# Performance work log

Measured on AMD Instinct MI355X. Metric: run time of the kernel, lower is better.

Reference implementation:

```python
import jax, jax.numpy as jnp
import numpy as np
from jax import lax

B, IMG, ED, NC = 32, 224, 256, 10
DI, DS, DC, DR = 512, 64, 4, 16   # d_inner, d_state, d_conv, dt_rank
NB, L = 6, (IMG // 16) ** 2       # 6 mamba blocks, seq len 196
EPS = 1e-5


def setup_inputs():
    key = jax.random.key(0)
    ks = iter(jax.random.split(key, 48))
    def rn(shape, s=0.02):
        return jax.random.normal(next(ks), shape, jnp.float32) * s
    def ru(shape):
        return jax.random.uniform(next(ks), shape, jnp.float32, 0.5, 1.5)
    inp = {"x": jax.random.normal(next(ks), (B, 3, IMG, IMG), jnp.float32)}
    c = [ED // 4, ED // 2, ED]
    for i, (ci, co) in enumerate([(3, c[0]), (c[0], c[1]), (c[1], c[2])], 1):
        inp[f"c{i}w"] = rn((co, ci, 3, 3), 0.05)
        inp[f"c{i}b"] = rn((co,))
        inp[f"b{i}g"] = jnp.ones((co,), jnp.float32)
        inp[f"b{i}b"] = jnp.zeros((co,), jnp.float32)
        inp[f"b{i}m"] = rn((co,))
        inp[f"b{i}v"] = ru((co,))
    inp["ln_g"] = jnp.ones((NB, ED), jnp.float32)
    inp["ln_b"] = jnp.zeros((NB, ED), jnp.float32)
    inp["w_in"] = rn((NB, 2 * DI, ED))
    inp["cw"] = rn((NB, DI, DC), 0.1)
    inp["cb"] = rn((NB, DI))
    inp["w_x"] = rn((NB, DR + 2 * DS, DI))
    inp["w_dt"] = rn((NB, DI, DR), 0.1)
    inp["b_dt"] = rn((NB, DI), 0.5)
    inp["a_log"] = jnp.tile(jnp.log(jnp.arange(1, DS + 1, dtype=jnp.float32)), (NB, DI, 1))
    inp["d_skip"] = jnp.ones((NB, DI), jnp.float32)
    inp["w_out"] = rn((NB, ED, DI))
    inp["fc_w"] = rn((NC, ED))
    inp["fc_b"] = jnp.zeros((NC,), jnp.float32)
    return inp


def _conv2d(x, w, s, p):
    return lax.conv_general_dilated(x, w, (s, s), [(p, p), (p, p)],
                                    dimension_numbers=("NCHW", "OIHW", "NCHW"))


def _bn(x, g, b, m, v):
    sh = (1, -1, 1, 1)
    return (x - m.reshape(sh)) * (g.reshape(sh) / jnp.sqrt(v.reshape(sh) + EPS)) + b.reshape(sh)


def _maxpool(x, k, s, p):
    return lax.reduce_window(x, -jnp.inf, lax.max, (1, 1, k, k), (1, 1, s, s),
                             [(0, 0), (0, 0), (p, p), (p, p)])


def _mamba_block(x, ln_g, ln_b, w_in, cw, cb, w_x, w_dt, b_dt, a_log, d_skip, w_out):
    res = x
    mu = x.mean(-1, keepdims=True)
    var = ((x - mu) ** 2).mean(-1, keepdims=True)
    h = (x - mu) / jnp.sqrt(var + EPS) * ln_g + ln_b
    xz = jnp.einsum("bld,ed->ble", h, w_in)            # [B,L,2*DI]
    xi, z = xz[..., :DI], xz[..., DI:]
    # causal depthwise conv1d (pad left DC-1) + silu
    xt = lax.conv_general_dilated(xi.transpose(0, 2, 1), cw[:, None, :], (1,),
                                  [(DC - 1, 0)], dimension_numbers=("NCH", "OIH", "NCH"),
                                  feature_group_count=DI) + cb[None, :, None]
    xc = jax.nn.silu(xt).transpose(0, 2, 1)            # [B,L,DI]
    dbl = jnp.einsum("bld,ed->ble", xc, w_x)           # [B,L,DR+2*DS]
    dt = jax.nn.softplus(jnp.einsum("blr,dr->bld", dbl[..., :DR], w_dt) + b_dt)
    Bm = dbl[..., DR:DR + DS]                          # [B,L,DS]
    Cm = dbl[..., DR + DS:]                            # [B,L,DS]
    A = -jnp.exp(a_log)                                # [DI,DS]

    def step(hst, ins):
        dt_t, b_t, c_t, x_t = ins                      # [B,DI],[B,DS],[B,DS],[B,DI]
        dA = jnp.exp(dt_t[..., None] * A)              # [B,DI,DS]
        hst = dA * hst + (dt_t * x_t)[..., None] * b_t[:, None, :]
        return hst, jnp.einsum("bds,bs->bd", hst, c_t)

    h0 = jnp.zeros((x.shape[0], DI, DS), x.dtype)
    _, ys = lax.scan(step, h0, (dt.transpose(1, 0, 2), Bm.transpose(1, 0, 2),
                                Cm.transpose(1, 0, 2), xc.transpose(1, 0, 2)))
    y = ys.transpose(1, 0, 2) + d_skip * xc
    y = y * jax.nn.silu(z)
    return jnp.einsum("bld,ed->ble", y, w_out) + res


def reference(x, c1w, c1b, b1g, b1b, b1m, b1v, c2w, c2b, b2g, b2b, b2m, b2v,
              c3w, c3b, b3g, b3b, b3m, b3v, ln_g, ln_b, w_in, cw, cb, w_x,
              w_dt, b_dt, a_log, d_skip, w_out, fc_w, fc_b):
    h = _maxpool(jax.nn.relu(_bn(_conv2d(x, c1w, 2, 1) + c1b.reshape(1, -1, 1, 1), b1g, b1b, b1m, b1v)), 3, 2, 1)
    h = _maxpool(jax.nn.relu(_bn(_conv2d(h, c2w, 1, 1) + c2b.reshape(1, -1, 1, 1), b2g, b2b, b2m, b2v)), 2, 2, 0)
    h = _maxpool(jax.nn.relu(_bn(_conv2d(h, c3w, 1, 1) + c3b.reshape(1, -1, 1, 1), b3g, b3b, b3m, b3v)), 2, 2, 0)
    h = h.reshape(h.shape[0], ED, -1).transpose(0, 2, 1)   # [B,L,ED]
    for i in range(NB):
        h = _mamba_block(h, ln_g[i], ln_b[i], w_in[i], cw[i], cb[i], w_x[i],
                         w_dt[i], b_dt[i], a_log[i], d_skip[i], w_out[i])
    h = h.mean(axis=1)                                     # adaptive avg pool over L
    return h @ fc_w.T + fc_b
```

## Files before the change

kernel.cpp:

```cpp
#include <hip/hip_runtime.h>

typedef __bf16 bf16x8 __attribute__((ext_vector_type(8)));
typedef float f32x4 __attribute__((ext_vector_type(4)));

#define EPS 1e-5f

__device__ __forceinline__ unsigned short f2bu(float f) {
  union { float f; unsigned u; } x; x.f = f;
  unsigned r = x.u + 0x7fffu + ((x.u >> 16) & 1u);
  return (unsigned short)(r >> 16);
}
__device__ __forceinline__ float bu2f(unsigned short u) {
  union { unsigned u; float f; } x; x.u = ((unsigned)u) << 16;
  return x.f;
}

__device__ __forceinline__ void gld16(const void* g, void* l) {
  __builtin_amdgcn_global_load_lds((const __attribute__((address_space(1))) void*)g,
                                   (__attribute__((address_space(3))) void*)l, 16, 0, 0);
}

__global__ __launch_bounds__(256) void k_prep(
    const float* __restrict__ w_in, unsigned short* __restrict__ w_in_bf,
    const float* __restrict__ w_x, unsigned short* __restrict__ w_x_bf,
    const float* __restrict__ w_out, unsigned short* __restrict__ w_out_bf,
    const float* __restrict__ c2w, unsigned short* __restrict__ w2p,
    const float* __restrict__ c3w, unsigned short* __restrict__ w3p,
    const float* __restrict__ w_dt, float* __restrict__ wdt_t) {
  int id = blockIdx.x * 256 + threadIdx.x;
  if (id < 1572864) { w_in_bf[id] = f2bu(w_in[id]); return; }
  id -= 1572864;
  if (id < 442368) { w_x_bf[id] = f2bu(w_x[id]); return; }
  id -= 442368;
  if (id < 786432) { w_out_bf[id] = f2bu(w_out[id]); return; }
  id -= 786432;
  if (id < 73728) {
    int ci = id % 64, tap = (id / 64) % 9, co = id / 576;
    w2p[id] = f2bu(c2w[(co * 64 + ci) * 9 + tap]);
    return;
  }
  id -= 73728;
  if (id < 294912) {
    int ci = id % 128, tap = (id / 128) % 9, co = id / 1152;
    w3p[id] = f2bu(c3w[(co * 128 + ci) * 9 + tap]);
    return;
  }
  id -= 294912;
  {
    int d = id & 511, r = (id >> 9) & 15, blk = id >> 13;
    wdt_t[id] = w_dt[(blk * 512 + d) * 16 + r];
  }
}

__global__ __launch_bounds__(256) void k_conv1a(
    const float* __restrict__ x, const float* __restrict__ w,
    const float* __restrict__ cb, const float* __restrict__ g,
    const float* __restrict__ bb, const float* __restrict__ bm_,
    const float* __restrict__ bv, unsigned short* __restrict__ out) {
  __shared__ float sw[64 * 27];
  __shared__ float sa[64], sb[64];
  for (int i = threadIdx.x; i < 64 * 27; i += 256) sw[i] = w[i];
  if (threadIdx.x < 64) {
    int c = threadIdx.x;
    float alpha = g[c] * rsqrtf(bv[c] + EPS);
    sa[c] = alpha;
    sb[c] = (cb[c] - bm_[c]) * alpha + bb[c];
  }
  __syncthreads();
  int id = blockIdx.x * 256 + threadIdx.x;
  int c = id & 63;
  int t = id >> 6;
  int ox = t % 112; t /= 112;
  int oy = t % 112;
  int b = t / 112;
  float wr[27];
#pragma unroll
  for (int i = 0; i < 27; ++i) wr[i] = sw[c * 27 + i];
  float alpha = sa[c], beta = sb[c];
  const float* base = x + (size_t)b * 3 * 224 * 224 + (oy * 2 - 1) * 224 + (ox * 2 - 1);
  float acc = 0.f;
  if (oy >= 1 && ox >= 1) {
#pragma unroll
    for (int ci = 0; ci < 3; ++ci)
#pragma unroll
      for (int ky = 0; ky < 3; ++ky)
#pragma unroll
        for (int kx = 0; kx < 3; ++kx)
          acc = fmaf(base[ci * 224 * 224 + ky * 224 + kx], wr[ci * 9 + ky * 3 + kx], acc);
  } else {
#pragma unroll
    for (int ci = 0; ci < 3; ++ci)
#pragma unroll
      for (int ky = 0; ky < 3; ++ky) {
        int iy = oy * 2 - 1 + ky;
        bool vy = (unsigned)iy < 224u;
#pragma unroll
        for (int kx = 0; kx < 3; ++kx) {
          int ix = ox * 2 - 1 + kx;
          float v = (vy && (unsigned)ix < 224u)
                        ? x[(size_t)b * 3 * 224 * 224 + (ci * 224 + iy) * 224 + ix] : 0.f;
          acc = fmaf(v, wr[ci * 9 + ky * 3 + kx], acc);
        }
      }
  }
  out[id] = f2bu(fmaxf(acc * alpha + beta, 0.f));
}

__global__ __launch_bounds__(256) void k_pool3(const unsigned short* __restrict__ in,
                                               unsigned short* __restrict__ out) {
  int id = blockIdx.x * 256 + threadIdx.x;
  int c = id & 63;
  int t = id >> 6;
  int px = t % 56; t /= 56;
  int py = t % 56;
  int b = t / 56;
  float m = 0.f;
#pragma unroll
  for (int ky = 0; ky < 3; ++ky) {
    int iy = py * 2 - 1 + ky;
    if ((unsigned)iy >= 112u) continue;
#pragma unroll
    for (int kx = 0; kx < 3; ++kx) {
      int ix = px * 2 - 1 + kx;
      if ((unsigned)ix >= 112u) continue;
      m = fmaxf(m, bu2f(in[(((size_t)(b * 112 + iy) * 112) + ix) * 64 + c]));
    }
  }
  out[id] = f2bu(m);
}

template <int H, int Wd, int CI, int CO>
__global__ __launch_bounds__(256) void k_convgemm(
    const unsigned short* __restrict__ In, const unsigned short* __restrict__ Wt,
    const float* __restrict__ cb, const float* __restrict__ g,
    const float* __restrict__ bb, const float* __restrict__ bm_,
    const float* __restrict__ bv, unsigned short* __restrict__ Out) {
  constexpr int K = 9 * CI;
  constexpr int NTN = CO / 64;
  int bm = blockIdx.x / NTN, bn = blockIdx.x - bm * NTN;
  int lane = threadIdx.x & 63, wid = threadIdx.x >> 6;
  int wr = wid >> 1, wc = wid & 1;
  int r0 = bm * 64 + wr * 32 + (lane & 15);
  int r1 = r0 + 16;
  int c0 = bn * 64 + wc * 32 + (lane & 15);
  int koff = (lane >> 4) << 3;
  int ox0 = r0 % Wd; int t0 = r0 / Wd; int oy0 = t0 % H; int b0 = t0 / H;
  int ox1 = r1 % Wd; int t1 = r1 / Wd; int oy1 = t1 % H; int b1 = t1 / H;
  const unsigned short* pb0 = Wt + (size_t)c0 * K + koff;
  const unsigned short* pb1 = Wt + (size_t)(c0 + 16) * K + koff;
  f32x4 acc[2][2] = {};
  for (int k0 = 0; k0 < K; k0 += 32) {
    int k = k0 + koff;
    int tap = k / CI;
    int ci = k - tap * CI;
    int ky = tap / 3, kx = tap - ky * 3;
    int iy0 = oy0 + ky - 1, ix0 = ox0 + kx - 1;
    int iy1 = oy1 + ky - 1, ix1 = ox1 + kx - 1;
    bf16x8 a0 = {};
    bf16x8 a1 = {};
    if ((unsigned)iy0 < (unsigned)H && (unsigned)ix0 < (unsigned)Wd)
      a0 = *(const bf16x8*)(In + ((size_t)((b0 * H + iy0) * Wd + ix0)) * CI + ci);
    if ((unsigned)iy1 < (unsigned)H && (unsigned)ix1 < (unsigned)Wd)
      a1 = *(const bf16x8*)(In + ((size_t)((b1 * H + iy1) * Wd + ix1)) * CI + ci);
    bf16x8 w0 = *(const bf16x8*)(pb0 + k0);
    bf16x8 w1 = *(const bf16x8*)(pb1 + k0);
    acc[0][0] = __builtin_amdgcn_mfma_f32_16x16x32_bf16(a0, w0, acc[0][0], 0, 0, 0);
    acc[0][1] = __builtin_amdgcn_mfma_f32_16x16x32_bf16(a0, w1, acc[0][1], 0, 0, 0);
    acc[1][0] = __builtin_amdgcn_mfma_f32_16x16x32_bf16(a1, w0, acc[1][0], 0, 0, 0);
    acc[1][1] = __builtin_amdgcn_mfma_f32_16x16x32_bf16(a1, w1, acc[1][1], 0, 0, 0);
  }
  int rr = (lane >> 4) * 4, rc = lane & 15;
#pragma unroll
  for (int tj = 0; tj < 2; ++tj) {
    int col = bn * 64 + wc * 32 + tj * 16 + rc;
    float alpha = g[col] * rsqrtf(bv[col] + EPS);
    float beta = (cb[col] - bm_[col]) * alpha + bb[col];
#pragma unroll
    for (int ti = 0; ti < 2; ++ti) {
      int row = bm * 64 + wr * 32 + ti * 16 + rr;
#pragma unroll
      for (int r = 0; r < 4; ++r) {
        float v = fmaxf(acc[ti][tj][r] * alpha + beta, 0.f);
        Out[(size_t)(row + r) * CO + col] = f2bu(v);
      }
    }
  }
}

template <int H, int Wd, int C, bool OUTF>
__global__ __launch_bounds__(256) void k_pool(const unsigned short* __restrict__ in,
                                              void* __restrict__ outv) {
  constexpr int OH = H / 2, OW = Wd / 2;
  int id = blockIdx.x * 256 + threadIdx.x;
  int c = id % C;
  int t = id / C;
  int px = t % OW; t /= OW;
  int py = t % OH;
  int b = t / OH;
  const unsigned short* p = in + (((size_t)(b * H + py * 2) * Wd) + px * 2) * C + c;
  float m0 = bu2f(p[0]), m1 = bu2f(p[C]);
  float m2 = bu2f(p[(size_t)Wd * C]), m3 = bu2f(p[(size_t)Wd * C + C]);
  float m = fmaxf(fmaxf(m0, m1), fmaxf(m2, m3));
  if (OUTF) ((float*)outv)[id] = m;
  else ((unsigned short*)outv)[id] = f2bu(m);
}

__global__ __launch_bounds__(256) void k_ln(const float* __restrict__ h,
                                            const float* __restrict__ g,
                                            const float* __restrict__ b2,
                                            unsigned short* __restrict__ out) {
  int lane = threadIdx.x & 63, wid = threadIdx.x >> 6;
  int t = blockIdx.x * 4 + wid;
  float4 v = *(const float4*)(h + (size_t)t * 256 + lane * 4);
  float s = v.x + v.y + v.z + v.w;
  float q = v.x * v.x + v.y * v.y + v.z * v.z + v.w * v.w;
#pragma unroll
  for (int off = 32; off; off >>= 1) {
    s += __shfl_xor(s, off);
    q += __shfl_xor(q, off);
  }
  float mu = s * (1.f / 256.f);
  float var = q * (1.f / 256.f) - mu * mu;
  float rs = rsqrtf(var + EPS);
  float4 gg = *(const float4*)(g + lane * 4);
  float4 bb = *(const float4*)(b2 + lane * 4);
  ushort4 o;
  o.x = f2bu((v.x - mu) * rs * gg.x + bb.x);
  o.y = f2bu((v.y - mu) * rs * gg.y + bb.y);
  o.z = f2bu((v.z - mu) * rs * gg.z + bb.z);
  o.w = f2bu((v.w - mu) * rs * gg.w + bb.w);
  *(ushort4*)(out + (size_t)t * 256 + lane * 4) = o;
}

template <int BM, int BN, int KSTEPS, bool ADD>
__global__ __launch_bounds__(256) void k_sgemm(const unsigned short* __restrict__ A,
                                               const unsigned short* __restrict__ W,
                                               float* __restrict__ C,
                                               int N, int ntn) {
  constexpr int K = KSTEPS * 64;
  constexpr int MR = BM / 32;
  constexpr int NR = BN / 32;
  __shared__ __align__(16) unsigned short As[BM * 64];
  __shared__ __align__(16) unsigned short Bs[BN * 64];
  int bm = blockIdx.x / ntn, bn = blockIdx.x - bm * ntn;
  int lane = threadIdx.x & 63, wid = threadIdx.x >> 6;
  int wr = wid >> 1, wc = wid & 1;
  const int arow = lane >> 3, acol = (lane & 7) * 8;
  f32x4 acc[MR][NR] = {};
  const unsigned short* Abase = A + (size_t)(bm * BM) * K;
  const unsigned short* Wbase = W + (size_t)(bn * BN) * K;
  for (int t = 0; t < KSTEPS; ++t) {
    int k0 = t * 64;
#pragma unroll
    for (int i = 0; i < BM / 32; ++i) {
      int chunk = wid * (BM / 32) + i;
      gld16(Abase + (size_t)(chunk * 8 + arow) * K + k0 + acol, &As[chunk * 512 + lane * 8]);
    }
#pragma unroll
    for (int i = 0; i < BN / 32; ++i) {
      int chunk = wid * (BN / 32) + i;
      gld16(Wbase + (size_t)(chunk * 8 + arow) * K + k0 + acol, &Bs[chunk * 512 + lane * 8]);
    }
    __syncthreads();
#pragma unroll
    for (int kk = 0; kk < 2; ++kk) {
      bf16x8 af[MR], bfr[NR];
#pragma unroll
      for (int mi = 0; mi < MR; ++mi)
        af[mi] = *(const bf16x8*)&As[(wr * (BM / 2) + mi * 16 + (lane & 15)) * 64 + kk * 32 + (lane >> 4) * 8];
#pragma unroll
      for (int nj = 0; nj < NR; ++nj)
        bfr[nj] = *(const bf16x8*)&Bs[(wc * (BN / 2) + nj * 16 + (lane & 15)) * 64 + kk * 32 + (lane >> 4) * 8];
#pragma unroll
      for (int mi = 0; mi < MR; ++mi)
#pragma unroll
        for (int nj = 0; nj < NR; ++nj)
          acc[mi][nj] = __builtin_amdgcn_mfma_f32_16x16x32_bf16(af[mi], bfr[nj], acc[mi][nj], 0, 0, 0);
    }
    __syncthreads();
  }
  int rr = (lane >> 4) * 4, rc = lane & 15;
#pragma unroll
  for (int mi = 0; mi < MR; ++mi)
#pragma unroll
    for (int nj = 0; nj < NR; ++nj) {
      int row = bm * BM + wr * (BM / 2) + mi * 16 + rr;
      int col = bn * BN + wc * (BN / 2) + nj * 16 + rc;
#pragma unroll
      for (int r = 0; r < 4; ++r) {
        float v = acc[mi][nj][r];
        if (ADD) v += C[(size_t)(row + r) * N + col];
        C[(size_t)(row + r) * N + col] = v;
      }
    }
}

template <bool ADD_RES>
__global__ __launch_bounds__(256) void k_gemm(const unsigned short* __restrict__ A,
                                              const unsigned short* __restrict__ W,
                                              float* __restrict__ C, int M, int N,
                                              int K, int ntn) {
  int bm = blockIdx.x / ntn, bn = blockIdx.x - bm * ntn;
  int lane = threadIdx.x & 63, wid = threadIdx.x >> 6;
  int wr = wid >> 1, wc = wid & 1;
  int r0 = bm * 64 + wr * 32 + (lane & 15);
  int c0 = bn * 64 + wc * 32 + (lane & 15);
  int koff = (lane >> 4) << 3;
  int cc0 = (c0 < N) ? c0 : (N - 1);
  int cc1 = (c0 + 16 < N) ? (c0 + 16) : (N - 1);
  const unsigned short* pa0 = A + (size_t)r0 * K + koff;
  const unsigned short* pa1 = A + (size_t)(r0 + 16) * K + koff;
  const unsigned short* pb0 = W + (size_t)cc0 * K + koff;
  const unsigned short* pb1 = W + (size_t)cc1 * K + koff;
  f32x4 acc[2][2] = {};
  for (int k0 = 0; k0 < K; k0 += 32) {
    bf16x8 a0 = *(const bf16x8*)(pa0 + k0);
    bf16x8 a1 = *(const bf16x8*)(pa1 + k0);
    bf16x8 b0 = *(const bf16x8*)(pb0 + k0);
    bf16x8 b1 = *(const bf16x8*)(pb1 + k0);
    acc[0][0] = __builtin_amdgcn_mfma_f32_16x16x32_bf16(a0, b0, acc[0][0], 0, 0, 0);
    acc[0][1] = __builtin_amdgcn_mfma_f32_16x16x32_bf16(a0, b1, acc[0][1], 0, 0, 0);
    acc[1][0] = __builtin_amdgcn_mfma_f32_16x16x32_bf16(a1, b0, acc[1][0], 0, 0, 0);
    acc[1][1] = __builtin_amdgcn_mfma_f32_16x16x32_bf16(a1, b1, acc[1][1], 0, 0, 0);
  }
  int rr = (lane >> 4) * 4, rc = lane & 15;
#pragma unroll
  for (int ti = 0; ti < 2; ++ti)
#pragma unroll
    for (int tj = 0; tj < 2; ++tj) {
      int col = bn * 64 + wc * 32 + tj * 16 + rc;
      if (col >= N) continue;
      int row = bm * 64 + wr * 32 + ti * 16 + rr;
#pragma unroll
      for (int r = 0; r < 4; ++r) {
        float v = acc[ti][tj][r];
        if (ADD_RES) v += C[(size_t)(row + r) * N + col];
        C[(size_t)(row + r) * N + col] = v;
      }
    }
}

__global__ __launch_bounds__(256) void k_dwconv(const float* __restrict__ xz,
                                                const float* __restrict__ cw,
                                                const float* __restrict__ cb,
                                                float* __restrict__ xc,
                                                unsigned short* __restrict__ xcb) {
  int id = blockIdx.x * 256 + threadIdx.x;
  int d = id & 511;
  int bl = id >> 9;
  int l = bl % 196;
  int b = bl / 196;
  const float* xi = xz + (size_t)(b * 196) * 1024 + d;
  float4 c4 = *(const float4*)(cw + d * 4);
  float acc = cb[d];
  if (l >= 3) acc = fmaf(xi[(size_t)(l - 3) * 1024], c4.x, acc);
  if (l >= 2) acc = fmaf(xi[(size_t)(l - 2) * 1024], c4.y, acc);
  if (l >= 1) acc = fmaf(xi[(size_t)(l - 1) * 1024], c4.z, acc);
  acc = fmaf(xi[(size_t)l * 1024], c4.w, acc);
  float s = acc / (1.f + __expf(-acc));
  xc[id] = s;
  xcb[id] = f2bu(s);
}

__global__ __launch_bounds__(256) void k_dt(const float* __restrict__ dbl,
                                            const float* __restrict__ wt,
                                            const float* __restrict__ bdt,
                                            float* __restrict__ dt) {
  int id = blockIdx.x * 256 + threadIdx.x;
  int d = id & 511;
  int bl = id >> 9;
  const float4* a = (const float4*)(dbl + (size_t)bl * 144);
  float acc = bdt[d];
#pragma unroll
  for (int i = 0; i < 4; ++i) {
    float4 av = a[i];
    acc = fmaf(av.x, wt[(i * 4 + 0) * 512 + d], acc);
    acc = fmaf(av.y, wt[(i * 4 + 1) * 512 + d], acc);
    acc = fmaf(av.z, wt[(i * 4 + 2) * 512 + d], acc);
    acc = fmaf(av.w, wt[(i * 4 + 3) * 512 + d], acc);
  }
  dt[id] = fmaxf(acc, 0.f) + log1pf(__expf(-fabsf(acc)));
}

__global__ __launch_bounds__(256) void k_scan(
    const float* __restrict__ dtb, const float* __restrict__ xc,
    const float* __restrict__ dbl, const float* __restrict__ xz,
    const float* __restrict__ a_log, const float* __restrict__ d_skip,
    unsigned short* __restrict__ y) {
  __shared__ float lds[4][584];
  int lane = threadIdx.x & 63, wid = threadIdx.x >> 6;
  int wgid = blockIdx.x * 4 + wid;
  int b = wgid >> 9, d = wgid & 511;
  float A = -__expf(a_log[d * 64 + lane]);
  float dsk = d_skip[d];
  const float* dt_p = dtb + (size_t)(b * 196) * 512 + d;
  const float* xc_p = xc + (size_t)(b * 196) * 512 + d;
  const float* z_p = xz + (size_t)(b * 196) * 1024 + 512 + d;
  const float* bc_p = dbl + (size_t)(b * 196) * 144 + 16 + lane;
  unsigned short* y_p = y + (size_t)(b * 196) * 512 + d;
  float* L = lds[wid];
  float h = 0.f;
  int g = lane >> 3, j = lane & 7;
  for (int l0 = 0; l0 < 196; l0 += 8) {
    float p[8];
#pragma unroll
    for (int li = 0; li < 8; ++li) {
      int l = l0 + li;
      bool ok = (l < 196);
      float dtv = ok ? dt_p[(size_t)l * 512] : 0.f;
      float xv = ok ? xc_p[(size_t)l * 512] : 0.f;
      float Bv = ok ? bc_p[(size_t)l * 144] : 0.f;
      float Cv = ok ? bc_p[(size_t)l * 144 + 64] : 0.f;
      float dA = __expf(dtv * A);
      h = fmaf(dA, h, (dtv * xv) * Bv);
      p[li] = h * Cv;
    }
#pragma unroll
    for (int li = 0; li < 8; ++li) L[lane * 9 + li] = p[li];
    __builtin_amdgcn_wave_barrier();
    float s = 0.f;
#pragma unroll
    for (int k = 0; k < 8; ++k) s += L[(j * 8 + k) * 9 + g];
    __builtin_amdgcn_wave_barrier();
    s += __shfl_xor(s, 1);
    s += __shfl_xor(s, 2);
    s += __shfl_xor(s, 4);
    int l = l0 + g;
    if (j == 0 && l < 196) {
      float xv = xc_p[(size_t)l * 512];
      float zv = z_p[(size_t)l * 1024];
      float sig = 1.f / (1.f + __expf(-zv));
      y_p[(size_t)l * 512] = f2bu((s + dsk * xv) * (zv * sig));
    }
  }
}

__global__ __launch_bounds__(256) void k_mean2(const float* __restrict__ h,
                                               float* __restrict__ part) {
  int b = blockIdx.x >> 2, q = blockIdx.x & 3;
  int e = threadIdx.x;
  const float* hb = h + ((size_t)b * 196 + q * 49) * 256 + e;
  float s = 0.f;
  for (int l = 0; l < 49; ++l) s += hb[(size_t)l * 256];
  part[((size_t)b * 4 + q) * 256 + e] = s;
}

__global__ __launch_bounds__(256) void k_head(const float* __restrict__ part,
                                              const float* __restrict__ fw,
                                              const float* __restrict__ fb,
                                              float* __restrict__ out) {
  __shared__ float sp[256];
  int b = blockIdx.x;
  int tid = threadIdx.x, lane = tid & 63, w = tid >> 6;
  const float* pb = part + (size_t)b * 4 * 256;
  sp[tid] = (pb[tid] + pb[256 + tid] + pb[512 + tid] + pb[768 + tid]) * (1.f / 196.f);
  __syncthreads();
  for (int n = w; n < 10; n += 4) {
    float s = 0.f;
#pragma unroll
    for (int i = 0; i < 4; ++i) {
      int e = lane * 4 + i;
      e = e & 255;
      s += sp[e] * fw[n * 256 + e];
    }
    s += __shfl_xor(s, 1); s += __shfl_xor(s, 2); s += __shfl_xor(s, 4);
    s += __shfl_xor(s, 8); s += __shfl_xor(s, 16); s += __shfl_xor(s, 32);
    if (lane == 0) out[b * 10 + n] = s + fb[n];
  }
}

static inline unsigned cdiv(unsigned a, unsigned b) { return (a + b - 1) / b; }

extern "C" void kernel_launch(void* const* d_in, const int* in_sizes, int n_in,
                              void* d_out, int out_size, void* d_ws, size_t ws_size,
                              hipStream_t stream) {
  const float* x = (const float*)d_in[0];
  const float* c1w = (const float*)d_in[1]; const float* c1b = (const float*)d_in[2];
  const float* b1g = (const float*)d_in[3]; const float* b1b = (const float*)d_in[4];
  const float* b1m = (const float*)d_in[5]; const float* b1v = (const float*)d_in[6];
  const float* c2w = (const float*)d_in[7]; const float* c2b = (const float*)d_in[8];
  const float* b2g = (const float*)d_in[9]; const float* b2b = (const float*)d_in[10];
  const float* b2m = (const float*)d_in[11]; const float* b2v = (const float*)d_in[12];
  const float* c3w = (const float*)d_in[13]; const float* c3b = (const float*)d_in[14];
  const float* b3g = (const float*)d_in[15]; const float* b3b = (const float*)d_in[16];
  const float* b3m = (const float*)d_in[17]; const float* b3v = (const float*)d_in[18];
  const float* ln_g = (const float*)d_in[19]; const float* ln_b = (const float*)d_in[20];
  const float* w_in = (const float*)d_in[21];
  const float* cw = (const float*)d_in[22]; const float* cbv = (const float*)d_in[23];
  const float* w_x = (const float*)d_in[24];
  const float* w_dt = (const float*)d_in[25]; const float* b_dt = (const float*)d_in[26];
  const float* a_log = (const float*)d_in[27]; const float* d_skip = (const float*)d_in[28];
  const float* w_out = (const float*)d_in[29];
  const float* fc_w = (const float*)d_in[30]; const float* fc_b = (const float*)d_in[31];

  char* ws = (char*)d_ws;
  size_t off = 0;
  auto take = [&](size_t bytes) { size_t o = off; off += bytes; return o; };
  size_t S = take(67837952);
  unsigned short* c1o = (unsigned short*)(ws + S + 0);
  unsigned short* t1 = (unsigned short*)(ws + S + 51380224);
  unsigned short* t2 = (unsigned short*)(ws + S + 0);
  unsigned short* t3 = (unsigned short*)(ws + S + 25690112);
  unsigned short* t4 = (unsigned short*)(ws + S + 32112640);
  float* xz = (float*)(ws + S + 0);
  float* xc = (float*)(ws + S + 25690112);
  unsigned short* xcb = (unsigned short*)(ws + S + 38535168);
  float* dbl = (float*)(ws + S + 44957696);
  float* dtb = (float*)(ws + S + 48570368);
  unsigned short* ybf = (unsigned short*)(ws + S + 61415424);
  float* h = (float*)(ws + take(6422528));
  unsigned short* hbf = (unsigned short*)(ws + take(3211264));
  unsigned short* w_in_bf = (unsigned short*)(ws + take(3145728));
  unsigned short* w_x_bf = (unsigned short*)(ws + take(884736));
  unsigned short* w_out_bf = (unsigned short*)(ws + take(1572864));
  unsigned short* w2p = (unsigned short*)(ws + take(147456));
  unsigned short* w3p = (unsigned short*)(ws + take(589824));
  float* wdt_t = (float*)(ws + take(196608));
  float* part = (float*)(ws + take(131072));
  (void)ws_size; (void)in_sizes; (void)n_in; (void)out_size;

  k_prep<<<12576, 256, 0, stream>>>(w_in, w_in_bf, w_x, w_x_bf, w_out, w_out_bf,
                                    c2w, w2p, c3w, w3p, w_dt, wdt_t);

  k_conv1a<<<100352, 256, 0, stream>>>(x, c1w, c1b, b1g, b1b, b1m, b1v, c1o);
  k_pool3<<<25088, 256, 0, stream>>>(c1o, t1);
  k_convgemm<56, 56, 64, 128><<<1568 * 2, 256, 0, stream>>>(t1, w2p, c2b, b2g, b2b, b2m, b2v, t2);
  k_pool<56, 56, 128, false><<<12544, 256, 0, stream>>>(t2, t3);
  k_convgemm<28, 28, 128, 256><<<392 * 4, 256, 0, stream>>>(t3, w3p, c3b, b3g, b3b, b3m, b3v, t4);
  k_pool<28, 28, 256, true><<<6272, 256, 0, stream>>>(t4, h);

  for (int blk = 0; blk < 6; ++blk) {
    k_ln<<<1568, 256, 0, stream>>>(h, ln_g + blk * 256, ln_b + blk * 256, hbf);
    k_sgemm<128, 128, 4, false><<<49 * 8, 256, 0, stream>>>(
        hbf, w_in_bf + (size_t)blk * 1024 * 256, xz, 1024, 8);
    k_dwconv<<<12544, 256, 0, stream>>>(xz, cw + blk * 512 * 4, cbv + blk * 512, xc, xcb);
    k_gemm<false><<<98 * 3, 256, 0, stream>>>(xcb, w_x_bf + (size_t)blk * 144 * 512, dbl,
                                              6272, 144, 512, 3);
    k_dt<<<12544, 256, 0, stream>>>(dbl, wdt_t + blk * 8192, b_dt + blk * 512, dtb);
    k_scan<<<4096, 256, 0, stream>>>(dtb, xc, dbl, xz, a_log + blk * 512 * 64,
                                     d_skip + blk * 512, ybf);
    k_sgemm<64, 64, 8, true><<<98 * 4, 256, 0, stream>>>(
        ybf, w_out_bf + (size_t)blk * 256 * 512, h, 256, 4);
  }

  k_mean2<<<128, 256, 0, stream>>>(h, part);
  k_head<<<32, 256, 0, stream>>>(part, fc_w, fc_b, (float*)d_out);
}
```

Measured before the change: 1.937 ms.

## Tile conv1 per output row with shared-memory input staging and register accumulation

The first 3x3 stride-2 convolution now runs one block per (batch, output row). The block stages the 9 padded input rows in shared memory, and each thread accumulates 28 output columns for one channel in registers using vectorized LDS reads. This replaces the old one-output-per-thread scheme, which re-read global input 27 times per output and launched about 100k blocks. The cost is higher register pressure from 28 accumulators and fewer blocks in flight. Output stores become strided by 64 channels per thread, but they stay coalesced across the channel lanes.

```diff
diff --git a/kernel.cpp b/kernel.cpp
--- a/kernel.cpp
+++ b/kernel.cpp
@@ -57,53 +57,65 @@
     const float* __restrict__ cb, const float* __restrict__ g,
     const float* __restrict__ bb, const float* __restrict__ bm_,
     const float* __restrict__ bv, unsigned short* __restrict__ out) {
+  __shared__ __align__(16) float sx[9][228];
   __shared__ float sw[64 * 27];
   __shared__ float sa[64], sb[64];
-  for (int i = threadIdx.x; i < 64 * 27; i += 256) sw[i] = w[i];
-  if (threadIdx.x < 64) {
-    int c = threadIdx.x;
+  int tid = threadIdx.x;
+  int oy = blockIdx.x % 112, b = blockIdx.x / 112;
+  for (int i = tid; i < 9 * 228; i += 256) {
+    int row = i / 228;
+    int ixl = i - row * 228;
+    int ci = row / 3, ky = row - ci * 3;
+    int iy = 2 * oy - 1 + ky;
+    int ix = ixl - 1;
+    float v = 0.f;
+    if ((unsigned)iy < 224u && (unsigned)ix < 224u)
+      v = x[((size_t)(b * 3 + ci) * 224 + iy) * 224 + ix];
+    sx[row][ixl] = v;
+  }
+  for (int i = tid; i < 64 * 27; i += 256) sw[i] = w[i];
+  if (tid < 64) {
+    int c = tid;
     float alpha = g[c] * rsqrtf(bv[c] + EPS);
     sa[c] = alpha;
     sb[c] = (cb[c] - bm_[c]) * alpha + bb[c];
   }
   __syncthreads();
-  int id = blockIdx.x * 256 + threadIdx.x;
-  int c = id & 63;
-  int t = id >> 6;
-  int ox = t % 112; t /= 112;
-  int oy = t % 112;
-  int b = t / 112;
-  float wr[27];
-#pragma unroll
-  for (int i = 0; i < 27; ++i) wr[i] = sw[c * 27 + i];
-  float alpha = sa[c], beta = sb[c];
-  const float* base = x + (size_t)b * 3 * 224 * 224 + (oy * 2 - 1) * 224 + (ox * 2 - 1);
-  float acc = 0.f;
-  if (oy >= 1 && ox >= 1) {
-#pragma unroll
-    for (int ci = 0; ci < 3; ++ci)
-#pragma unroll
-      for (int ky = 0; ky < 3; ++ky)
-#pragma unroll
-        for (int kx = 0; kx < 3; ++kx)
-          acc = fmaf(base[ci * 224 * 224 + ky * 224 + kx], wr[ci * 9 + ky * 3 + kx], acc);
-  } else {
-#pragma unroll
-    for (int ci = 0; ci < 3; ++ci)
-#pragma unroll
-      for (int ky = 0; ky < 3; ++ky) {
-        int iy = oy * 2 - 1 + ky;
-        bool vy = (unsigned)iy < 224u;
-#pragma unroll
-        for (int kx = 0; kx < 3; ++kx) {
-          int ix = ox * 2 - 1 + kx;
-          float v = (vy && (unsigned)ix < 224u)
-                        ? x[(size_t)b * 3 * 224 * 224 + (ci * 224 + iy) * 224 + ix] : 0.f;
-          acc = fmaf(v, wr[ci * 9 + ky * 3 + kx], acc);
+  int c = tid & 63, grp = tid >> 6;
+  int ox0 = grp * 28;
+  float acc[28];
+#pragma unroll
+  for (int i = 0; i < 28; ++i) acc[i] = 0.f;
+#pragma unroll
+  for (int ci = 0; ci < 3; ++ci) {
+    float wr[9];
+#pragma unroll
+    for (int j = 0; j < 9; ++j) wr[j] = sw[c * 27 + ci * 9 + j];
+#pragma unroll
+    for (int ky = 0; ky < 3; ++ky) {
+      const float* row = sx[ci * 3 + ky];
+#pragma unroll
+      for (int q = 0; q < 7; ++q) {
+        int base = 2 * (ox0 + q * 4);
+        f32x4 a0 = *(const f32x4*)&row[base];
+        f32x4 a1 = *(const f32x4*)&row[base + 4];
+        f32x4 a2 = *(const f32x4*)&row[base + 8];
+        float xv[12] = {a0[0], a0[1], a0[2], a0[3], a1[0], a1[1],
+                        a1[2], a1[3], a2[0], a2[1], a2[2], a2[3]};
+#pragma unroll
+        for (int p = 0; p < 4; ++p) {
+          acc[q * 4 + p] = fmaf(xv[2 * p + 0], wr[ky * 3 + 0], acc[q * 4 + p]);
+          acc[q * 4 + p] = fmaf(xv[2 * p + 1], wr[ky * 3 + 1], acc[q * 4 + p]);
+          acc[q * 4 + p] = fmaf(xv[2 * p + 2], wr[ky * 3 + 2], acc[q * 4 + p]);
         }
       }
-  }
-  out[id] = f2bu(fmaxf(acc * alpha + beta, 0.f));
+    }
+  }
+  float alpha = sa[c], beta = sb[c];
+  unsigned short* op = out + (((size_t)(b * 112 + oy)) * 112 + ox0) * 64 + c;
+#pragma unroll
+  for (int p = 0; p < 28; ++p)
+    op[(size_t)p * 64] = f2bu(fmaxf(acc[p] * alpha + beta, 0.f));
 }
 
 __global__ __launch_bounds__(256) void k_pool3(const unsigned short* __restrict__ in,
@@ -522,7 +534,7 @@
   k_prep<<<12576, 256, 0, stream>>>(w_in, w_in_bf, w_x, w_x_bf, w_out, w_out_bf,
                                     c2w, w2p, c3w, w3p, w_dt, wdt_t);
 
-  k_conv1a<<<100352, 256, 0, stream>>>(x, c1w, c1b, b1g, b1b, b1m, b1v, c1o);
+  k_conv1a<<<3584, 256, 0, stream>>>(x, c1w, c1b, b1g, b1b, b1m, b1v, c1o);
   k_pool3<<<25088, 256, 0, stream>>>(c1o, t1);
   k_convgemm<56, 56, 64, 128><<<1568 * 2, 256, 0, stream>>>(t1, w2p, c2b, b2g, b2b, b2m, b2v, t2);
   k_pool<56, 56, 128, false><<<12544, 256, 0, stream>>>(t2, t3);
```

After: 1.770 ms. -8.7%, faster.
